# Optimization experiments

Hardware: AMD Instinct MI355X
Metric: run time of the kernel (lower is better)

Reference implementation:

```python
import jax, jax.numpy as jnp
import numpy as np

NUM_FEATURES = 4
LATENT = 16
HIDDEN = 128
N_PIECES = 20
B, P = 8192, 128


def setup_inputs() -> dict:
    key = jax.random.key(0)
    ks = jax.random.split(key, 8)
    s = lambda fan_in: 1.0 / np.sqrt(fan_in)
    return {
        "x": jax.random.normal(ks[0], (B, P * NUM_FEATURES), jnp.float32),
        "W1": jax.random.normal(ks[1], (NUM_FEATURES, HIDDEN), jnp.float32) * s(NUM_FEATURES),
        "b1": jnp.zeros((HIDDEN,), jnp.float32),
        "W2": jax.random.normal(ks[2], (HIDDEN, HIDDEN), jnp.float32) * s(HIDDEN),
        "b2": jnp.zeros((HIDDEN,), jnp.float32),
        "W3": jax.random.normal(ks[3], (HIDDEN, 2 * LATENT), jnp.float32) * s(HIDDEN),
        "b3": jnp.zeros((2 * LATENT,), jnp.float32),
        "pool_weight": jax.random.normal(ks[4], (2 * LATENT, N_PIECES + 1), jnp.float32) * 0.1,
        "eps": jax.random.normal(ks[5], (B, LATENT), jnp.float32),
    }


def _fspool_weights(pool_weight, set_size):
    # piecewise-linear interpolation of pool_weight over normalized rank positions
    pos = jnp.arange(set_size, dtype=jnp.float32) / (set_size - 1) * N_PIECES  # [P]
    idx = jnp.clip(pos.astype(jnp.int32), 0, N_PIECES)
    frac = pos - idx.astype(jnp.float32)
    left = pool_weight[:, idx]                                   # [C, P]
    right = pool_weight[:, jnp.clip(idx + 1, 0, N_PIECES)]       # [C, P]
    return (1.0 - frac) * left + frac * right                    # [C, P]


def reference(x, W1, b1, W2, b2, W3, b3, pool_weight, eps):
    # per-particle shared MLP, batched over particles (B, P, F) -> (B, P, 2L)
    h = x.reshape(B, P, NUM_FEATURES)
    h = jax.nn.relu(jnp.einsum("bpf,fh->bph", h, W1) + b1)
    h = jax.nn.relu(jnp.einsum("bph,hk->bpk", h, W2) + b2)
    h = jnp.einsum("bph,hc->bpc", h, W3) + b3                    # [B, P, 2L]
    z = jnp.transpose(h, (0, 2, 1))                              # [B, 2L, P]
    # FSPool: descending featurewise sort + rank-weighted sum over set dim
    z_sorted = jnp.flip(jnp.sort(z, axis=-1), axis=-1)           # [B, 2L, P]
    w = _fspool_weights(pool_weight, P)                          # [2L, P]
    pooled = jnp.sum(z_sorted * w[None], axis=-1)                # [B, 2L]
    mus = pooled[:, ::2]
    logvars = pooled[:, 1::2]
    samples = mus + eps * jnp.exp(0.5 * logvars)
    return (mus, logvars, samples)
```

## Files before the change

### kernel.cpp

```cpp
#include <hip/hip_runtime.h>

#define B_TOT 8192
#define NB    16
#define NPCS  20

typedef __attribute__((ext_vector_type(8))) __fp16 f16x8;
typedef __attribute__((ext_vector_type(4))) float f32x4;
typedef __attribute__((ext_vector_type(2))) __fp16 fp16x2;

__device__ __forceinline__ unsigned pkmax(unsigned a, unsigned b) {
    unsigned d; asm("v_pk_max_f16 %0, %1, %2" : "=v"(d) : "v"(a), "v"(b)); return d;
}
__device__ __forceinline__ unsigned pkmin(unsigned a, unsigned b) {
    unsigned d; asm("v_pk_min_f16 %0, %1, %2" : "=v"(d) : "v"(a), "v"(b)); return d;
}
__device__ __forceinline__ unsigned pkrne(float a, float b) {
    fp16x2 h;
    h.x = (__fp16)a;
    h.y = (__fp16)b;
    return __builtin_bit_cast(unsigned, h);
}
__device__ __forceinline__ unsigned pkrtz(float a, float b) {
    return __builtin_bit_cast(unsigned, __builtin_amdgcn_cvt_pkrtz(a, b));
}
__device__ __forceinline__ float asf(unsigned u) { return __builtin_bit_cast(float, u); }
__device__ __forceinline__ unsigned asu(float f) { return __builtin_bit_cast(unsigned, f); }
__device__ __forceinline__ fp16x2 ash2(unsigned u) { return __builtin_bit_cast(fp16x2, u); }
__device__ __forceinline__ unsigned asu2(fp16x2 h) { return __builtin_bit_cast(unsigned, h); }

template<int CTRL>
__device__ __forceinline__ unsigned dppmov(unsigned v) {
    return (unsigned)__builtin_amdgcn_mov_dpp((int)v, CTRL, 0xf, 0xf, true);
}
__device__ __forceinline__ unsigned xlane(unsigned v, int lm) {
    switch (lm) {
    case 1:  return dppmov<0xB1>(v);
    case 2:  return dppmov<0x4E>(v);
    case 4:  return (unsigned)__builtin_amdgcn_ds_swizzle((int)v, 0x101F);
    default: return dppmov<0x128>(v);
    }
}
__device__ __forceinline__ float xlanef(float v, int lm) { return asf(xlane(asu(v), lm)); }

#define WS_W3T 32768
#define WS_WSP 40960
#define WS_W1A 57344
#define WS_B1F 61440

__device__ __forceinline__ unsigned packh2(float lo, float hi) {
    unsigned short a = __builtin_bit_cast(unsigned short, (__fp16)lo);
    unsigned short b = __builtin_bit_cast(unsigned short, (__fp16)hi);
    return (unsigned)a | ((unsigned)b << 16);
}

__device__ __forceinline__ int piperm(int j) {
    return (j & 0x60) | ((j & 0x0C) << 1) | ((j & 0x10) >> 2) | (j & 3);
}

__global__ void prep_kernel(const float* __restrict__ W1, const float* __restrict__ b1,
                            const float* __restrict__ W2, const float* __restrict__ W3,
                            const float* __restrict__ pw, void* __restrict__ ws)
{
    const int t = blockIdx.x * 256 + threadIdx.x;
    __fp16* w2t = (__fp16*)ws;
    __fp16* w3t = (__fp16*)((char*)ws + WS_W3T);
    float* wsp  = (float*)((char*)ws + WS_WSP);
    unsigned* w1a = (unsigned*)((char*)ws + WS_W1A);
    unsigned* b1f = (unsigned*)((char*)ws + WS_B1F);
    if (t < 16384) {
        int j = t >> 7, k = t & 127;
        w2t[t] = (__fp16)W2[k * 128 + piperm(j)];
    } else if (t < 20480) {
        int o = t - 16384, c = o >> 7, k = o & 127;
        w3t[o] = (__fp16)W3[k * 32 + c];
    } else if (t < 24576) {
        int o = t - 20480, c = o >> 7, p = o & 127;
        float pos = (float)p * (20.0f / 127.0f);
        int ip = min((int)pos, NPCS);
        float fr = pos - (float)ip;
        int ipb = min(ip + 1, NPCS);
        wsp[o] = (1.0f - fr) * pw[c * 21 + ip] + fr * pw[c * 21 + ipb];
    } else if (t < 25600) {
        int idx = t - 24576;
        int ht = idx >> 7, lane = (idx >> 1) & 63, pair = idx & 1;
        int quad = lane >> 4, l16 = lane & 15;
        unsigned val = 0;
        if (quad == 0) {
            int sh = piperm(16 * ht + l16);
            val = packh2(W1[(2 * pair) * 128 + sh], W1[(2 * pair + 1) * 128 + sh]);
        }
        w1a[idx] = val;
    } else if (t < 26112) {
        int idx = t - 25600;
        int ht = idx >> 6, lane = idx & 63;
        int quad = lane >> 4, l16 = lane & 15;
        unsigned val = 0;
        if (quad == 0) {
            int sh = piperm(16 * ht + l16);
            val = packh2(b1[sh], 0.0f);
        }
        b1f[idx] = val;
    }
}

#define L_SZP  32768
#define L_POOL 41216

__global__ __launch_bounds__(256, 2) void enc_kernel(
    const float* __restrict__ x,   const float* __restrict__ b1g,
    const float* __restrict__ b2g, const float* __restrict__ b3g,
    const float* __restrict__ eps, const void* __restrict__ ws,
    float* __restrict__ out)
{
    __shared__ __align__(16) char smem[43264];

    const int tid  = threadIdx.x;
    const int wv   = tid >> 6;
    const int lane = tid & 63;
    const int l16  = lane & 15;
    const int quad = lane >> 4;
    const int b0   = blockIdx.x * NB;

    {
        const uint4* src = (const uint4*)ws;
#pragma unroll
        for (int it = 0; it < 8; ++it) {
            int idx = tid + it * 256;
            int j = idx >> 4, ch = idx & 15;
            *(uint4*)(smem + j * 256 + ((ch ^ (j & 15)) * 16)) = src[idx];
        }
    }

    f16x8 w3f[2][4];
    {
        const __fp16* w3t = (const __fp16*)((const char*)ws + WS_W3T);
#pragma unroll
        for (int mt2 = 0; mt2 < 2; ++mt2)
#pragma unroll
            for (int kt = 0; kt < 4; ++kt)
                w3f[mt2][kt] = *(const f16x8*)(w3t + (mt2 * 16 + l16) * 128 + kt * 32 + quad * 8);
    }
    union WF { unsigned u[4]; f16x8 v; } w1f[8];
    {
        const unsigned* w1a = (const unsigned*)((const char*)ws + WS_W1A);
        const unsigned* b1f = (const unsigned*)((const char*)ws + WS_B1F);
#pragma unroll
        for (int ht = 0; ht < 8; ++ht) {
            uint2 w01 = *(const uint2*)(w1a + ht * 128 + lane * 2);
            w1f[ht].u[0] = w01.x;
            w1f[ht].u[1] = w01.y;
            w1f[ht].u[2] = b1f[ht * 64 + lane];
            w1f[ht].u[3] = 0;
        }
    }
    f32x4 b3acc[2];
    {
        float4 t0 = *(const float4*)(b3g + quad * 4);
        float4 t1 = *(const float4*)(b3g + 16 + quad * 4);
        b3acc[0] = (f32x4){t0.x, t0.y, t0.z, t0.w};
        b3acc[1] = (f32x4){t1.x, t1.y, t1.z, t1.w};
    }
    f32x4 b2acc[8];
#pragma unroll
    for (int nt = 0; nt < 8; ++nt) {
        float4 t4 = *(const float4*)(b2g + (nt >> 1) * 32 + quad * 8 + (nt & 1) * 4);
        b2acc[nt] = (f32x4){t4.x, t4.y, t4.z, t4.w};
    }

    const int pr = wv * 4 + quad;
    float wE[8], wO[8];
    {
        const float* wsp = (const float*)((const char*)ws + WS_WSP);
        float4 e0 = *(const float4*)(wsp + (2 * pr) * 128 + l16 * 8);
        float4 e1 = *(const float4*)(wsp + (2 * pr) * 128 + l16 * 8 + 4);
        float4 o0 = *(const float4*)(wsp + (2 * pr + 1) * 128 + l16 * 8);
        float4 o1 = *(const float4*)(wsp + (2 * pr + 1) * 128 + l16 * 8 + 4);
        wE[0]=e0.x; wE[1]=e0.y; wE[2]=e0.z; wE[3]=e0.w; wE[4]=e1.x; wE[5]=e1.y; wE[6]=e1.z; wE[7]=e1.w;
        wO[0]=o0.x; wO[1]=o0.y; wO[2]=o0.z; wO[3]=o0.w; wO[4]=o1.x; wO[5]=o1.y; wO[6]=o1.z; wO[7]=o1.w;
    }

    const int ib = l16 * 8;
    const unsigned sfl8  = (ib & 8)  ? 0x80008000u : 0u;
    const unsigned sfl16 = (ib & 16) ? 0x80008000u : 0u;
    const unsigned sfl32 = (ib & 32) ? 0x80008000u : 0u;
    const unsigned sfl64 = (ib & 64) ? 0x80008000u : 0u;

    __syncthreads();

    unsigned* szp   = (unsigned*)(smem + L_SZP);
    float*    spool = (float*)(smem + L_POOL);

    union XB { unsigned u[4]; f16x8 v; } xb0, xb1;
    xb0.u[2] = 0x3C003C00u; xb0.u[3] = 0;
    xb1.u[2] = 0x3C003C00u; xb1.u[3] = 0;
    const f32x4 zc = (f32x4){0.f, 0.f, 0.f, 0.f};

    const float* xptr = x + (size_t)b0 * 512 + (wv * 32 + l16) * 4;
    float4 xv0 = *(const float4*)(xptr);
    float4 xv1 = *(const float4*)(xptr + 64);

    for (int e = 0; e < NB; ++e) {
        xb0.u[0] = pkrtz(xv0.x, xv0.y);
        xb0.u[1] = pkrtz(xv0.z, xv0.w);
        xb1.u[0] = pkrtz(xv1.x, xv1.y);
        xb1.u[1] = pkrtz(xv1.z, xv1.w);

        if (e + 1 < NB) {
            xv0 = *(const float4*)(xptr + (e + 1) * 512);
            xv1 = *(const float4*)(xptr + (e + 1) * 512 + 64);
        }

        union AF { unsigned u[4]; f16x8 v; } a1[2][4];
#pragma unroll
        for (int ht = 0; ht < 8; ++ht) {
            f32x4 d0 = __builtin_amdgcn_mfma_f32_16x16x32_f16(w1f[ht].v, xb0.v, zc, 0, 0, 0);
            f32x4 d1 = __builtin_amdgcn_mfma_f32_16x16x32_f16(w1f[ht].v, xb1.v, zc, 0, 0, 0);
            const int kt = ht >> 1, jb = 2 * (ht & 1);
            a1[0][kt].u[jb]     = pkmax(pkrtz(d0[0], d0[1]), 0u);
            a1[0][kt].u[jb + 1] = pkmax(pkrtz(d0[2], d0[3]), 0u);
            a1[1][kt].u[jb]     = pkmax(pkrtz(d1[0], d1[1]), 0u);
            a1[1][kt].u[jb + 1] = pkmax(pkrtz(d1[2], d1[3]), 0u);
        }

        f32x4 acc2[2][8];
#pragma unroll
        for (int kt = 0; kt < 4; ++kt)
#pragma unroll
            for (int nt = 0; nt < 8; ++nt) {
                const int j = nt * 16 + l16;
                const int phys = (kt * 4 + quad) ^ l16;
                f16x8 wf = *(const f16x8*)(smem + j * 256 + phys * 16);
                if (kt == 0) {
                    acc2[0][nt] = __builtin_amdgcn_mfma_f32_16x16x32_f16(wf, a1[0][0].v, b2acc[nt], 0, 0, 0);
                    acc2[1][nt] = __builtin_amdgcn_mfma_f32_16x16x32_f16(wf, a1[1][0].v, b2acc[nt], 0, 0, 0);
                } else {
                    acc2[0][nt] = __builtin_amdgcn_mfma_f32_16x16x32_f16(wf, a1[0][kt].v, acc2[0][nt], 0, 0, 0);
                    acc2[1][nt] = __builtin_amdgcn_mfma_f32_16x16x32_f16(wf, a1[1][kt].v, acc2[1][nt], 0, 0, 0);
                }
            }

#pragma unroll
        for (int mt = 0; mt < 2; ++mt) {
            unsigned pkx[8], pky[8];
#pragma unroll
            for (int nt = 0; nt < 8; ++nt) {
                pkx[nt] = pkmax(pkrtz(acc2[mt][nt][0], acc2[mt][nt][1]), 0u);
                pky[nt] = pkmax(pkrtz(acc2[mt][nt][2], acc2[mt][nt][3]), 0u);
            }
            union A3 { unsigned u[4]; f16x8 v; } a3[4];
#pragma unroll
            for (int kt = 0; kt < 4; ++kt) {
                a3[kt].u[0] = pkx[2 * kt];
                a3[kt].u[1] = pky[2 * kt];
                a3[kt].u[2] = pkx[2 * kt + 1];
                a3[kt].u[3] = pky[2 * kt + 1];
            }

            const int colbase = wv * 32 + mt * 16;
#pragma unroll
            for (int mt2 = 0; mt2 < 2; ++mt2) {
                f32x4 acc = __builtin_amdgcn_mfma_f32_16x16x32_f16(w3f[mt2][0], a3[0].v, b3acc[mt2], 0, 0, 0);
#pragma unroll
                for (int kt = 1; kt < 4; ++kt)
                    acc = __builtin_amdgcn_mfma_f32_16x16x32_f16(w3f[mt2][kt], a3[kt].v, acc, 0, 0, 0);
                const int prw = 8 * mt2 + 2 * quad;
                szp[prw * 132 + colbase + l16]       = pkrne(acc[0], acc[1]);
                szp[(prw + 1) * 132 + colbase + l16] = pkrne(acc[2], acc[3]);
            }
        }
        __syncthreads();

        unsigned v[8];
        {
            const unsigned* zp = szp + pr * 132 + l16 * 8;
            uint4 za = *(const uint4*)zp;
            uint4 zb = *(const uint4*)(zp + 4);
            v[0]=za.x; v[1]=za.y; v[2]=za.z; v[3]=za.w;
            v[4]=zb.x; v[5]=zb.y; v[6]=zb.z; v[7]=zb.w;
        }
#pragma unroll
        for (int k = 2; k <= 128; k <<= 1) {
#pragma unroll
            for (int j = 64; j >= 1; j >>= 1) {
                if (j >= k) continue;
                if (j >= 8) {
                    const bool km = ((ib & k) == 0) != ((ib & j) != 0);
                    const int lm = j >> 3;
#pragma unroll
                    for (int r = 0; r < 8; ++r) {
                        unsigned p = xlane(v[r], lm);
                        unsigned mx = pkmax(v[r], p), mn = pkmin(v[r], p);
                        v[r] = km ? mx : mn;
                    }
                } else if (k <= 4) {
#pragma unroll
                    for (int a = 0; a < 8; ++a) {
                        if (a & j) continue;
                        const int bx = a | j;
                        unsigned mx = pkmax(v[a], v[bx]), mn = pkmin(v[a], v[bx]);
                        if ((a & k) == 0) { v[a] = mx; v[bx] = mn; }
                        else              { v[a] = mn; v[bx] = mx; }
                    }
                } else {
                    const unsigned sfl = (k == 8) ? sfl8 : (k == 16) ? sfl16 :
                                         (k == 32) ? sfl32 : (k == 64) ? sfl64 : 0u;
                    if (j == 4 && k != 128) {
#pragma unroll
                        for (int r = 0; r < 8; ++r) v[r] ^= sfl;
                    }
#pragma unroll
                    for (int a = 0; a < 8; ++a) {
                        if (a & j) continue;
                        const int bx = a | j;
                        unsigned mx = pkmax(v[a], v[bx]), mn = pkmin(v[a], v[bx]);
                        v[a] = mx; v[bx] = mn;
                    }
                    if (j == 1 && k != 128) {
#pragma unroll
                        for (int r = 0; r < 8; ++r) v[r] ^= sfl;
                    }
                }
            }
        }

        float sE = 0.f, sO = 0.f;
#pragma unroll
        for (int r = 0; r < 8; ++r) {
            const fp16x2 hv = ash2(v[r]);
            sE = fmaf(wE[r], (float)hv.x, sE);
            sO = fmaf(wO[r], (float)hv.y, sO);
        }
#pragma unroll
        for (int d = 8; d >= 1; d >>= 1) {
            sE += xlanef(sE, d);
            sO += xlanef(sO, d);
        }
        if (l16 == 0) {
            spool[e * 32 + 2 * pr]     = sE;
            spool[e * 32 + 2 * pr + 1] = sO;
        }
        __syncthreads();
    }

    {
        const int e = tid >> 4, t = tid & 15;
        const float mu = spool[e * 32 + 2 * t];
        const float lv = spool[e * 32 + 2 * t + 1];
        const float ev = eps[(size_t)b0 * 16 + tid];
        const float smp = fmaf(ev, __expf(0.5f * lv), mu);
        out[(size_t)b0 * 16 + tid] = mu;
        out[(size_t)B_TOT * 16 + (size_t)b0 * 16 + tid] = lv;
        out[(size_t)2 * B_TOT * 16 + (size_t)b0 * 16 + tid] = smp;
    }
}

extern "C" void kernel_launch(void* const* d_in, const int* in_sizes, int n_in,
                              void* d_out, int out_size, void* d_ws, size_t ws_size,
                              hipStream_t stream) {
    const float* x   = (const float*)d_in[0];
    const float* W1  = (const float*)d_in[1];
    const float* b1  = (const float*)d_in[2];
    const float* W2  = (const float*)d_in[3];
    const float* b2  = (const float*)d_in[4];
    const float* W3  = (const float*)d_in[5];
    const float* b3  = (const float*)d_in[6];
    const float* pw  = (const float*)d_in[7];
    const float* eps = (const float*)d_in[8];
    float* out = (float*)d_out;

    prep_kernel<<<dim3(102), dim3(256), 0, stream>>>(W1, b1, W2, W3, pw, d_ws);
    enc_kernel<<<dim3(B_TOT / NB), dim3(256), 0, stream>>>(x, b1, b2, b3, eps, d_ws, out);
}
```

Measured before the change: 144.9 us.

## Double-buffer z staging to overlap MLP GEMMs with sort and drop a barrier

Splits the per-event loop into a GEMM phase and a sort/pool phase, and double-buffers the shared-memory z tile. The GEMMs for event e+1 now run before the sort of event e, and only one barrier per iteration is needed instead of two. This is meant to let MFMA work and the VALU-heavy bitonic sort interleave, and to cut synchronization stalls. In exchange shared memory grows by about 8 KB, which may affect the two-blocks-per-CU occupancy target, and register pressure may rise. The final prefetch re-reads the last row redundantly.

```diff
diff --git a/kernel.cpp b/kernel.cpp
--- a/kernel.cpp
+++ b/kernel.cpp
@@ -103,8 +103,9 @@
     }
 }
 
-#define L_SZP  32768
-#define L_POOL 41216
+#define L_SZP0 32768
+#define L_SZP1 41216
+#define L_POOL 49664
 
 __global__ __launch_bounds__(256, 2) void enc_kernel(
     const float* __restrict__ x,   const float* __restrict__ b1g,
@@ -112,7 +113,7 @@
     const float* __restrict__ eps, const void* __restrict__ ws,
     float* __restrict__ out)
 {
-    __shared__ __align__(16) char smem[43264];
+    __shared__ __align__(16) char smem[51712];
 
     const int tid  = threadIdx.x;
     const int wv   = tid >> 6;
@@ -187,7 +188,8 @@
 
     __syncthreads();
 
-    unsigned* szp   = (unsigned*)(smem + L_SZP);
+    unsigned* szpA  = (unsigned*)(smem + L_SZP0);
+    unsigned* szpB  = (unsigned*)(smem + L_SZP1);
     float*    spool = (float*)(smem + L_POOL);
 
     union XB { unsigned u[4]; f16x8 v; } xb0, xb1;
@@ -199,16 +201,15 @@
     float4 xv0 = *(const float4*)(xptr);
     float4 xv1 = *(const float4*)(xptr + 64);
 
-    for (int e = 0; e < NB; ++e) {
+    auto do_gemms = [&](unsigned* __restrict__ szpW, int pfIdx) {
         xb0.u[0] = pkrtz(xv0.x, xv0.y);
         xb0.u[1] = pkrtz(xv0.z, xv0.w);
         xb1.u[0] = pkrtz(xv1.x, xv1.y);
         xb1.u[1] = pkrtz(xv1.z, xv1.w);
 
-        if (e + 1 < NB) {
-            xv0 = *(const float4*)(xptr + (e + 1) * 512);
-            xv1 = *(const float4*)(xptr + (e + 1) * 512 + 64);
-        }
+        const int pfc = pfIdx < NB - 1 ? pfIdx : NB - 1;
+        xv0 = *(const float4*)(xptr + pfc * 512);
+        xv1 = *(const float4*)(xptr + pfc * 512 + 64);
 
         union AF { unsigned u[4]; f16x8 v; } a1[2][4];
 #pragma unroll
@@ -255,7 +256,6 @@
                 a3[kt].u[2] = pkx[2 * kt + 1];
                 a3[kt].u[3] = pky[2 * kt + 1];
             }
-
             const int colbase = wv * 32 + mt * 16;
 #pragma unroll
             for (int mt2 = 0; mt2 < 2; ++mt2) {
@@ -264,15 +264,16 @@
                 for (int kt = 1; kt < 4; ++kt)
                     acc = __builtin_amdgcn_mfma_f32_16x16x32_f16(w3f[mt2][kt], a3[kt].v, acc, 0, 0, 0);
                 const int prw = 8 * mt2 + 2 * quad;
-                szp[prw * 132 + colbase + l16]       = pkrne(acc[0], acc[1]);
-                szp[(prw + 1) * 132 + colbase + l16] = pkrne(acc[2], acc[3]);
-            }
-        }
-        __syncthreads();
-
+                szpW[prw * 132 + colbase + l16]       = pkrne(acc[0], acc[1]);
+                szpW[(prw + 1) * 132 + colbase + l16] = pkrne(acc[2], acc[3]);
+            }
+        }
+    };
+
+    auto do_sort = [&](const unsigned* __restrict__ szpR, int e) {
         unsigned v[8];
         {
-            const unsigned* zp = szp + pr * 132 + l16 * 8;
+            const unsigned* zp = szpR + pr * 132 + l16 * 8;
             uint4 za = *(const uint4*)zp;
             uint4 zb = *(const uint4*)(zp + 4);
             v[0]=za.x; v[1]=za.y; v[2]=za.z; v[3]=za.w;
@@ -339,8 +340,20 @@
             spool[e * 32 + 2 * pr]     = sE;
             spool[e * 32 + 2 * pr + 1] = sO;
         }
+    };
+
+    do_gemms(szpA, 1);
+    __syncthreads();
+
+    for (int e = 0; e < NB - 1; ++e) {
+        unsigned* srd = (e & 1) ? szpB : szpA;
+        unsigned* dwr = (e & 1) ? szpA : szpB;
+        do_gemms(dwr, e + 2);
+        do_sort(srd, e);
         __syncthreads();
     }
+    do_sort(((NB - 1) & 1) ? szpB : szpA, NB - 1);
+    __syncthreads();
 
     {
         const int e = tid >> 4, t = tid & 15;
```

Result: no change. 145.7 us (+0.6%).
